# Kernel optimization log

Hardware: AMD Instinct MI355X
Metric: run time of the kernel (lower is better)

The kernel has to match this reference:

```python
import jax, jax.numpy as jnp
import numpy as np

B, T, K, H = 256, 64, 49, 512


def setup_inputs() -> dict:
    key = jax.random.key(0)
    ks = jax.random.split(key, 7)
    s = 0.02
    return {
        "V": jax.random.normal(ks[0], (B, K, H), dtype=jnp.float32),
        "h_t": jax.random.normal(ks[1], (B, T, H), dtype=jnp.float32),
        "s_t": jax.random.normal(ks[2], (B, T, H), dtype=jnp.float32),
        "Wv": jax.random.normal(ks[3], (K, H), dtype=jnp.float32) * s,  # affine_v.weight [49, hidden]
        "Wg": jax.random.normal(ks[4], (K, H), dtype=jnp.float32) * s,  # affine_g.weight
        "Ws": jax.random.normal(ks[5], (K, H), dtype=jnp.float32) * s,  # affine_s.weight
        "Wh": jax.random.normal(ks[6], (1, K), dtype=jnp.float32) * s,  # affine_h.weight [1, 49]
    }


def reference(V, h_t, s_t, Wv, Wg, Ws, Wh):
    # Dropout is identity (inference / eval mode).
    content_v = jnp.einsum('bkh,ah->bka', V, Wv)      # [B,K,49]
    content_g = jnp.einsum('bth,ah->bta', h_t, Wg)    # [B,T,49]
    # broadcast add -> [B,T,K,49], tanh, project 49->1
    z_t = jnp.einsum('btka,a->btk',
                     jnp.tanh(content_g[:, :, None, :] + content_v[:, None, :, :]),
                     Wh[0])                            # [B,T,K]
    alpha_t = jax.nn.softmax(z_t, axis=-1)             # softmax over K regions
    c_t = jnp.einsum('btk,bkh->bth', alpha_t, V)       # [B,T,H]
    content_s = jnp.einsum('bth,ah->bta', s_t, Ws) + content_g  # [B,T,49]
    z_ext = jnp.einsum('bta,a->bt', jnp.tanh(content_s), Wh[0])[:, :, None]  # [B,T,1]
    extended = jnp.concatenate([z_t, z_ext], axis=2)   # [B,T,K+1]
    alpha_hat = jax.nn.softmax(extended, axis=-1)
    beta_t = alpha_hat[:, :, -1:]                      # [B,T,1] sentinel gate
    c_hat_t = beta_t * s_t + (1.0 - beta_t) * c_t      # [B,T,H]
    return (c_hat_t, alpha_t, beta_t)
```

## Files before the change

### kernel.cpp

```cpp
#include <hip/hip_runtime.h>
#include <hip/hip_bf16.h>
#include <math.h>

#define Bn 256
#define Tn 64
#define Kn 49
#define Hn 512
#define An 49

#define WS_CV 0
#define WS_CG 614656
#define WS_CS 1417472

#define OUT_ALPHA 8388608
#define OUT_BETA  9191424

typedef __attribute__((ext_vector_type(8))) short short8;
typedef __attribute__((ext_vector_type(4))) short short4v;
typedef __attribute__((ext_vector_type(4))) float f32x4;

#define WLDS 520

__device__ __forceinline__ short bfc(float x) {
    __hip_bfloat16 h = __float2bfloat16(x);
    return __builtin_bit_cast(short, h);
}

__device__ __forceinline__ float fast_tanh(float x) {
    float e = __expf(2.0f * x);
    return 1.0f - 2.0f / (e + 1.0f);
}

__global__ __launch_bounds__(256) void gemm3_mfma(
    const float* __restrict__ V, const float* __restrict__ h_t,
    const float* __restrict__ s_t, const float* __restrict__ Wv,
    const float* __restrict__ Wg, const float* __restrict__ Ws,
    float* __restrict__ ws)
{
    const int b = blockIdx.x;
    const int part = blockIdx.y;

    const float* A;
    const float* W;
    float* out;
    int R;
    if (part == 0)      { A = V   + (size_t)b*Kn*Hn; W = Wv; out = ws + WS_CV + (size_t)b*Kn*An; R = Kn; }
    else if (part == 1) { A = h_t + (size_t)b*Tn*Hn; W = Wg; out = ws + WS_CG + (size_t)b*Tn*An; R = Tn; }
    else                { A = s_t + (size_t)b*Tn*Hn; W = Ws; out = ws + WS_CS + (size_t)b*Tn*An; R = Tn; }

    __shared__ short Wl[Kn * WLDS];

    const int tid = threadIdx.x;

    for (int i = tid; i < Kn * 128; i += 256) {
        const int row = i >> 7;
        const int c4  = (i & 127) << 2;
        float4 v = *(const float4*)(W + (size_t)row * Hn + c4);
        short4v s;
        s.x = bfc(v.x); s.y = bfc(v.y); s.z = bfc(v.z); s.w = bfc(v.w);
        *(short4v*)(&Wl[row * WLDS + c4]) = s;
    }
    __syncthreads();

    const int wave = tid >> 6;
    const int lane = tid & 63;
    const int l15  = lane & 15;
    const int kgrp = lane >> 4;
    const int koff = kgrp * 8;

    const int r0 = wave * 16;
    int arow = r0 + l15; if (arow >= R) arow = R - 1;
    const float* Ap = A + (size_t)arow * Hn + koff;

    int brow[4];
    #pragma unroll
    for (int ct = 0; ct < 4; ++ct) {
        int r = ct * 16 + l15;
        brow[ct] = (r < Kn) ? r : (Kn - 1);
    }

    f32x4 acc[4] = {{0,0,0,0},{0,0,0,0},{0,0,0,0},{0,0,0,0}};

    for (int ks = 0; ks < 16; ++ks) {
        float4 a0 = *(const float4*)(Ap + ks * 32);
        float4 a1 = *(const float4*)(Ap + ks * 32 + 4);
        short8 af;
        af[0] = bfc(a0.x); af[1] = bfc(a0.y); af[2] = bfc(a0.z); af[3] = bfc(a0.w);
        af[4] = bfc(a1.x); af[5] = bfc(a1.y); af[6] = bfc(a1.z); af[7] = bfc(a1.w);
        #pragma unroll
        for (int ct = 0; ct < 4; ++ct) {
            short8 bfr = *(const short8*)(&Wl[brow[ct] * WLDS + koff + ks * 32]);
            acc[ct] = __builtin_amdgcn_mfma_f32_16x16x32_bf16(af, bfr, acc[ct], 0, 0, 0);
        }
    }

    #pragma unroll
    for (int ct = 0; ct < 4; ++ct) {
        const int a = ct * 16 + l15;
        if (a >= An) continue;
        #pragma unroll
        for (int i = 0; i < 4; ++i) {
            const int k = r0 + kgrp * 4 + i;
            if (k < R) out[(size_t)k * An + a] = acc[ct][i];
        }
    }
}

#define TT 16
__global__ __launch_bounds__(256) void fused_kernel(
    const float* __restrict__ V, const float* __restrict__ s_t,
    const float* __restrict__ Wh, const float* __restrict__ ws,
    float* __restrict__ out)
{
    const int bid = blockIdx.x;
    const int b  = bid >> 2;
    const int t0 = (bid & 3) * TT;

    __shared__ float cv[Kn][Kn];
    __shared__ float gl[TT][Kn];
    __shared__ float cl[TT][Kn];
    __shared__ float wh[Kn];
    __shared__ float zl[TT][Kn + 1];
    __shared__ float al[TT][Kn];
    __shared__ float bl[TT];

    const int tid = threadIdx.x;

    {
        const float* cvg = ws + WS_CV + (size_t)b * Kn * An;
        float* cvf = &cv[0][0];
        for (int i = tid; i < Kn * An; i += 256) cvf[i] = cvg[i];
        const float* cgg = ws + WS_CG + ((size_t)b * Tn + t0) * An;
        const float* csg = ws + WS_CS + ((size_t)b * Tn + t0) * An;
        float* gf = &gl[0][0];
        float* cf = &cl[0][0];
        for (int i = tid; i < TT * An; i += 256) { gf[i] = cgg[i]; cf[i] = csg[i]; }
        if (tid < An) wh[tid] = Wh[tid];
    }
    __syncthreads();

    for (int idx = tid; idx < TT * Kn + TT; idx += 256) {
        if (idx < TT * Kn) {
            const int tt = idx / Kn;
            const int k  = idx % Kn;
            float acc = 0.f;
            #pragma unroll 7
            for (int a = 0; a < Kn; ++a)
                acc += fast_tanh(gl[tt][a] + cv[k][a]) * wh[a];
            zl[tt][k] = acc;
        } else {
            const int tt = idx - TT * Kn;
            float acc = 0.f;
            #pragma unroll 7
            for (int a = 0; a < Kn; ++a)
                acc += fast_tanh(gl[tt][a] + cl[tt][a]) * wh[a];
            zl[tt][Kn] = acc;
        }
    }
    __syncthreads();

    {
        const int w    = tid >> 6;
        const int lane = tid & 63;
        for (int rr = 0; rr < 4; ++rr) {
            const int row = w * 4 + rr;
            float v = (lane < Kn) ? zl[row][lane] : -1e30f;
            float m = v;
            #pragma unroll
            for (int o = 32; o; o >>= 1) m = fmaxf(m, __shfl_xor(m, o, 64));
            float e = (lane < Kn) ? __expf(v - m) : 0.f;
            float s = e;
            #pragma unroll
            for (int o = 32; o; o >>= 1) s += __shfl_xor(s, o, 64);
            const float ze  = zl[row][Kn];
            const float m2  = fmaxf(m, ze);
            const float eze = __expf(ze - m2);
            const float denom = s * __expf(m - m2) + eze;
            const float beta  = eze / denom;
            if (lane < Kn) {
                const float a = e / s;
                al[row][lane] = a;
                out[OUT_ALPHA + ((size_t)(b * Tn + t0 + row)) * Kn + lane] = a;
            }
            if (lane == 0) {
                bl[row] = beta;
                out[OUT_BETA + (b * Tn + t0 + row)] = beta;
            }
        }
    }
    __syncthreads();

    {
        const int tt  = tid >> 4;
        const int l16 = tid & 15;
        const float* vb = V + (size_t)b * Kn * Hn;
        float4 acc[8] = {};
        for (int k = 0; k < Kn; ++k) {
            const float ak = al[tt][k];
            const float4* vr = (const float4*)(vb + (size_t)k * Hn);
            #pragma unroll
            for (int j = 0; j < 8; ++j) {
                float4 vv = vr[l16 + 16 * j];
                acc[j].x += ak * vv.x; acc[j].y += ak * vv.y;
                acc[j].z += ak * vv.z; acc[j].w += ak * vv.w;
            }
        }
        const float beta = bl[tt];
        const float omb  = 1.f - beta;
        const float4* sr = (const float4*)(s_t + ((size_t)b * Tn + t0 + tt) * Hn);
        float4* orow = (float4*)(out + ((size_t)b * Tn + t0 + tt) * Hn);
        #pragma unroll
        for (int j = 0; j < 8; ++j) {
            float4 sv = sr[l16 + 16 * j];
            float4 o;
            o.x = beta * sv.x + omb * acc[j].x;
            o.y = beta * sv.y + omb * acc[j].y;
            o.z = beta * sv.z + omb * acc[j].z;
            o.w = beta * sv.w + omb * acc[j].w;
            orow[l16 + 16 * j] = o;
        }
    }
}

extern "C" void kernel_launch(void* const* d_in, const int* in_sizes, int n_in,
                              void* d_out, int out_size, void* d_ws, size_t ws_size,
                              hipStream_t stream)
{
    const float* V   = (const float*)d_in[0];
    const float* h_t = (const float*)d_in[1];
    const float* s_t = (const float*)d_in[2];
    const float* Wv  = (const float*)d_in[3];
    const float* Wg  = (const float*)d_in[4];
    const float* Ws  = (const float*)d_in[5];
    const float* Wh  = (const float*)d_in[6];
    float* out = (float*)d_out;
    float* ws  = (float*)d_ws;

    dim3 g1(Bn, 3);
    gemm3_mfma<<<g1, 256, 0, stream>>>(V, h_t, s_t, Wv, Wg, Ws, ws);
    fused_kernel<<<Bn * 4, 256, 0, stream>>>(V, s_t, Wh, ws, out);
}
```

Baseline: 213.0 us.

## Factor tanh via precomputed exponentials and restructure context weighted-sum loop

The GEMM epilogue now stores exp(2x) of each projection, so the fused kernel computes tanh(g+v) as 1-2/(Eg*Ev+1) with one multiply and a hardware reciprocal per term, dropping the per-element exp. The sentinel term likewise uses the product Eg*Es. The sum over Wh is folded in by precomputing sum(Wh). LDS rows are padded to 52 for float4 reads, softmax divisions become rcp, and the context accumulation is reorganized so each thread owns two H columns across all 16 time rows, reading V once per block. Risks include exp overflow for large projections (inf gives rcp 0, which stays correct) and the reduced precision of approximate reciprocals.

Measured after the change: 175.2 us. -17.8%, faster.

```diff
diff --git a/kernel.cpp b/kernel.cpp
--- a/kernel.cpp
+++ b/kernel.cpp
@@ -8,9 +8,9 @@
 #define Hn 512
 #define An 49
 
-#define WS_CV 0
-#define WS_CG 614656
-#define WS_CS 1417472
+#define WS_EV 0
+#define WS_EG 614656
+#define WS_ES 1417472
 
 #define OUT_ALPHA 8388608
 #define OUT_BETA  9191424
@@ -24,11 +24,6 @@
 __device__ __forceinline__ short bfc(float x) {
     __hip_bfloat16 h = __float2bfloat16(x);
     return __builtin_bit_cast(short, h);
-}
-
-__device__ __forceinline__ float fast_tanh(float x) {
-    float e = __expf(2.0f * x);
-    return 1.0f - 2.0f / (e + 1.0f);
 }
 
 __global__ __launch_bounds__(256) void gemm3_mfma(
@@ -44,9 +39,9 @@
     const float* W;
     float* out;
     int R;
-    if (part == 0)      { A = V   + (size_t)b*Kn*Hn; W = Wv; out = ws + WS_CV + (size_t)b*Kn*An; R = Kn; }
-    else if (part == 1) { A = h_t + (size_t)b*Tn*Hn; W = Wg; out = ws + WS_CG + (size_t)b*Tn*An; R = Tn; }
-    else                { A = s_t + (size_t)b*Tn*Hn; W = Ws; out = ws + WS_CS + (size_t)b*Tn*An; R = Tn; }
+    if (part == 0)      { A = V   + (size_t)b*Kn*Hn; W = Wv; out = ws + WS_EV + (size_t)b*Kn*An; R = Kn; }
+    else if (part == 1) { A = h_t + (size_t)b*Tn*Hn; W = Wg; out = ws + WS_EG + (size_t)b*Tn*An; R = Tn; }
+    else                { A = s_t + (size_t)b*Tn*Hn; W = Ws; out = ws + WS_ES + (size_t)b*Tn*An; R = Tn; }
 
     __shared__ short Wl[Kn * WLDS];
 
@@ -101,12 +96,14 @@
         #pragma unroll
         for (int i = 0; i < 4; ++i) {
             const int k = r0 + kgrp * 4 + i;
-            if (k < R) out[(size_t)k * An + a] = acc[ct][i];
+            if (k < R) out[(size_t)k * An + a] = __expf(2.0f * acc[ct][i]);
         }
     }
 }
 
 #define TT 16
+#define AP 52
+
 __global__ __launch_bounds__(256) void fused_kernel(
     const float* __restrict__ V, const float* __restrict__ s_t,
     const float* __restrict__ Wh, const float* __restrict__ ws,
@@ -116,45 +113,89 @@
     const int b  = bid >> 2;
     const int t0 = (bid & 3) * TT;
 
-    __shared__ float cv[Kn][Kn];
-    __shared__ float gl[TT][Kn];
-    __shared__ float cl[TT][Kn];
-    __shared__ float wh[Kn];
+    __shared__ float EvL[Kn * AP];
+    __shared__ float EgL[TT * AP];
+    __shared__ float EcL[TT * AP];
+    __shared__ float whL[AP];
     __shared__ float zl[TT][Kn + 1];
-    __shared__ float al[TT][Kn];
+    __shared__ float al[TT][AP];
     __shared__ float bl[TT];
+    __shared__ float swhL;
 
     const int tid = threadIdx.x;
 
     {
-        const float* cvg = ws + WS_CV + (size_t)b * Kn * An;
-        float* cvf = &cv[0][0];
-        for (int i = tid; i < Kn * An; i += 256) cvf[i] = cvg[i];
-        const float* cgg = ws + WS_CG + ((size_t)b * Tn + t0) * An;
-        const float* csg = ws + WS_CS + ((size_t)b * Tn + t0) * An;
-        float* gf = &gl[0][0];
-        float* cf = &cl[0][0];
-        for (int i = tid; i < TT * An; i += 256) { gf[i] = cgg[i]; cf[i] = csg[i]; }
-        if (tid < An) wh[tid] = Wh[tid];
-    }
-    __syncthreads();
+        const float* evg = ws + WS_EV + (size_t)b * Kn * An;
+        for (int i = tid; i < Kn * An; i += 256) {
+            const int r = i / An;
+            const int c = i - r * An;
+            EvL[r * AP + c] = evg[i];
+        }
+        const float* egg = ws + WS_EG + ((size_t)b * Tn + t0) * An;
+        const float* esg = ws + WS_ES + ((size_t)b * Tn + t0) * An;
+        for (int i = tid; i < TT * An; i += 256) {
+            const int r = i / An;
+            const int c = i - r * An;
+            const float eg = egg[i];
+            EgL[r * AP + c] = eg;
+            EcL[r * AP + c] = eg * esg[i];
+        }
+        if (tid < Kn * 3) {
+            const int r = tid / 3;
+            const int c = An + (tid - r * 3);
+            EvL[r * AP + c] = 1.f;
+        }
+        if (tid >= 64 && tid < 64 + TT * 3) {
+            const int j = tid - 64;
+            const int r = j / 3;
+            const int c = An + (j - r * 3);
+            EgL[r * AP + c] = 1.f;
+            EcL[r * AP + c] = 1.f;
+        }
+        float whv = 0.f;
+        if (tid < AP) { whv = (tid < An) ? Wh[tid] : 0.f; whL[tid] = whv; }
+        if (tid < 64) {
+            float sv = whv;
+            #pragma unroll
+            for (int o = 32; o; o >>= 1) sv += __shfl_xor(sv, o, 64);
+            if (tid == 0) swhL = sv;
+        }
+    }
+    __syncthreads();
+
+    const float swh = swhL;
 
     for (int idx = tid; idx < TT * Kn + TT; idx += 256) {
         if (idx < TT * Kn) {
             const int tt = idx / Kn;
-            const int k  = idx % Kn;
+            const int k  = idx - tt * Kn;
+            const float4* eg4 = (const float4*)&EgL[tt * AP];
+            const float4* ev4 = (const float4*)&EvL[k * AP];
+            const float4* wh4 = (const float4*)whL;
             float acc = 0.f;
-            #pragma unroll 7
-            for (int a = 0; a < Kn; ++a)
-                acc += fast_tanh(gl[tt][a] + cv[k][a]) * wh[a];
-            zl[tt][k] = acc;
+            #pragma unroll
+            for (int j = 0; j < 13; ++j) {
+                const float4 g = eg4[j], v = ev4[j], w = wh4[j];
+                acc += w.x * __builtin_amdgcn_rcpf(g.x * v.x + 1.f);
+                acc += w.y * __builtin_amdgcn_rcpf(g.y * v.y + 1.f);
+                acc += w.z * __builtin_amdgcn_rcpf(g.z * v.z + 1.f);
+                acc += w.w * __builtin_amdgcn_rcpf(g.w * v.w + 1.f);
+            }
+            zl[tt][k] = swh - 2.f * acc;
         } else {
             const int tt = idx - TT * Kn;
+            const float4* ec4 = (const float4*)&EcL[tt * AP];
+            const float4* wh4 = (const float4*)whL;
             float acc = 0.f;
-            #pragma unroll 7
-            for (int a = 0; a < Kn; ++a)
-                acc += fast_tanh(gl[tt][a] + cl[tt][a]) * wh[a];
-            zl[tt][Kn] = acc;
+            #pragma unroll
+            for (int j = 0; j < 13; ++j) {
+                const float4 c = ec4[j], w = wh4[j];
+                acc += w.x * __builtin_amdgcn_rcpf(c.x + 1.f);
+                acc += w.y * __builtin_amdgcn_rcpf(c.y + 1.f);
+                acc += w.z * __builtin_amdgcn_rcpf(c.z + 1.f);
+                acc += w.w * __builtin_amdgcn_rcpf(c.w + 1.f);
+            }
+            zl[tt][Kn] = swh - 2.f * acc;
         }
     }
     __syncthreads();
@@ -162,6 +203,7 @@
     {
         const int w    = tid >> 6;
         const int lane = tid & 63;
+        #pragma unroll
         for (int rr = 0; rr < 4; ++rr) {
             const int row = w * 4 + rr;
             float v = (lane < Kn) ? zl[row][lane] : -1e30f;
@@ -176,12 +218,11 @@
             const float m2  = fmaxf(m, ze);
             const float eze = __expf(ze - m2);
             const float denom = s * __expf(m - m2) + eze;
-            const float beta  = eze / denom;
-            if (lane < Kn) {
-                const float a = e / s;
-                al[row][lane] = a;
+            const float beta  = eze * __builtin_amdgcn_rcpf(denom);
+            const float a = e * __builtin_amdgcn_rcpf(s);
+            if (lane < AP) al[row][lane] = a;
+            if (lane < Kn)
                 out[OUT_ALPHA + ((size_t)(b * Tn + t0 + row)) * Kn + lane] = a;
-            }
             if (lane == 0) {
                 bl[row] = beta;
                 out[OUT_BETA + (b * Tn + t0 + row)] = beta;
@@ -191,33 +232,37 @@
     __syncthreads();
 
     {
-        const int tt  = tid >> 4;
-        const int l16 = tid & 15;
-        const float* vb = V + (size_t)b * Kn * Hn;
-        float4 acc[8] = {};
-        for (int k = 0; k < Kn; ++k) {
-            const float ak = al[tt][k];
-            const float4* vr = (const float4*)(vb + (size_t)k * Hn);
-            #pragma unroll
-            for (int j = 0; j < 8; ++j) {
-                float4 vv = vr[l16 + 16 * j];
-                acc[j].x += ak * vv.x; acc[j].y += ak * vv.y;
-                acc[j].z += ak * vv.z; acc[j].w += ak * vv.w;
-            }
-        }
-        const float beta = bl[tt];
-        const float omb  = 1.f - beta;
-        const float4* sr = (const float4*)(s_t + ((size_t)b * Tn + t0 + tt) * Hn);
-        float4* orow = (float4*)(out + ((size_t)b * Tn + t0 + tt) * Hn);
-        #pragma unroll
-        for (int j = 0; j < 8; ++j) {
-            float4 sv = sr[l16 + 16 * j];
-            float4 o;
-            o.x = beta * sv.x + omb * acc[j].x;
-            o.y = beta * sv.y + omb * acc[j].y;
-            o.z = beta * sv.z + omb * acc[j].z;
-            o.w = beta * sv.w + omb * acc[j].w;
-            orow[l16 + 16 * j] = o;
+        const float2* vb2 = (const float2*)(V + (size_t)b * Kn * Hn);
+        float2 acc2[TT];
+        #pragma unroll
+        for (int r = 0; r < TT; ++r) { acc2[r].x = 0.f; acc2[r].y = 0.f; }
+
+        for (int j = 0; j < 13; ++j) {
+            const int k0 = j * 4;
+            float2 vv[4];
+            #pragma unroll
+            for (int u = 0; u < 4; ++u) {
+                int kk = k0 + u; kk = (kk > Kn - 1) ? (Kn - 1) : kk;
+                vv[u] = vb2[(size_t)kk * (Hn / 2) + tid];
+            }
+            #pragma unroll
+            for (int r = 0; r < TT; ++r) {
+                const float4 a4 = *(const float4*)&al[r][k0];
+                acc2[r].x += a4.x * vv[0].x + a4.y * vv[1].x + a4.z * vv[2].x + a4.w * vv[3].x;
+                acc2[r].y += a4.x * vv[0].y + a4.y * vv[1].y + a4.z * vv[2].y + a4.w * vv[3].y;
+            }
+        }
+
+        #pragma unroll
+        for (int r = 0; r < TT; ++r) {
+            const float beta = bl[r];
+            const float omb  = 1.f - beta;
+            const size_t row = (size_t)(b * Tn + t0 + r) * Hn;
+            const float2 sv = *(const float2*)(s_t + row + 2 * tid);
+            float2 o;
+            o.x = beta * sv.x + omb * acc2[r].x;
+            o.y = beta * sv.y + omb * acc2[r].y;
+            *(float2*)(out + row + 2 * tid) = o;
         }
     }
 }
```
